# Performance work log

Hardware: AMD Instinct MI355X
Metric: run time of the kernel (lower is better)

Reference implementation:

```python
import jax, jax.numpy as jnp
import numpy as np

GROUPS = 8
MAX_DISP = 24
EPS = 1e-5


def group_norm(x, gamma, beta, groups):
    B, C = x.shape[0], x.shape[1]
    spatial = x.shape[2:]
    xg = x.reshape(B, groups, C // groups, -1)
    mean = xg.mean(axis=(2, 3), keepdims=True)
    var = xg.var(axis=(2, 3), keepdims=True)
    xn = ((xg - mean) * jax.lax.rsqrt(var + EPS)).reshape(B, C, *spatial)
    shp = (1, C) + (1,) * len(spatial)
    return xn * gamma.reshape(shp) + beta.reshape(shp)


def conv3d(x, w):
    return jax.lax.conv_general_dilated(x, w, (1, 1, 1), [(1, 1)] * 3,
                                        dimension_numbers=("NCDHW", "OIDHW", "NCDHW"))


def conv2d(x, w):
    return jax.lax.conv_general_dilated(x, w, (1, 1), [(1, 1)] * 2,
                                        dimension_numbers=("NCHW", "OIHW", "NCHW"))


def conv1d(x, w):
    return jax.lax.conv_general_dilated(x, w, (1,), [(1, 1)],
                                        dimension_numbers=("NCW", "OIW", "NCW"))


def setup_inputs() -> dict:
    key = jax.random.key(0)
    ks = jax.random.split(key, 12)
    B, C, H, W = 2, 64, 160, 320
    feat_out = 16
    fL = jax.random.normal(ks[0], (B, C, H, W), dtype=jnp.float32)
    fR = jax.random.normal(ks[1], (B, C, H, W), dtype=jnp.float32)
    def w(k, shape):
        fan_in = int(np.prod(shape[1:]))
        return jax.random.normal(k, shape, dtype=jnp.float32) / np.sqrt(fan_in)
    return {
        "fL": fL, "fR": fR,
        # agg: Conv3d(groups->16) GN SiLU, Conv3d(16->16) GN SiLU, Conv3d(16->1)+bias
        "agg_w1": w(ks[2], (16, GROUPS, 3, 3, 3)),
        "agg_g1": jnp.ones((16,), jnp.float32), "agg_b1": jnp.zeros((16,), jnp.float32),
        "agg_w2": w(ks[3], (16, 16, 3, 3, 3)),
        "agg_g2": jnp.ones((16,), jnp.float32), "agg_b2": jnp.zeros((16,), jnp.float32),
        "agg_w3": w(ks[4], (1, 16, 3, 3, 3)), "agg_bias3": jnp.zeros((1,), jnp.float32),
        # feat_head: Conv2d(C->feat_out) GN SiLU
        "feat_w": w(ks[5], (feat_out, C, 3, 3)),
        "feat_g": jnp.ones((feat_out,), jnp.float32), "feat_b": jnp.zeros((feat_out,), jnp.float32),
        # apc_d: Conv1d(max_disp->max_disp, k=3, no bias)
        "apc_w": w(ks[6], (MAX_DISP, MAX_DISP, 3)),
        "reg_w1": w(ks[7], (32, MAX_DISP + feat_out, 3, 3)),
        "reg_g1": jnp.ones((32,), jnp.float32), "reg_b1": jnp.zeros((32,), jnp.float32),
        "reg_w2": w(ks[8], (1, 32, 3, 3)), "reg_bias2": jnp.zeros((1,), jnp.float32),
    }


def reference(fL, fR, agg_w1, agg_g1, agg_b1, agg_w2, agg_g2, agg_b2,
              agg_w3, agg_bias3, feat_w, feat_g, feat_b, apc_w,
              reg_w1, reg_g1, reg_b1, reg_w2, reg_bias2):
    B, C, H, W = fL.shape
    G, D = GROUPS, MAX_DISP
    cg = C // G
    fL_g = fL.reshape(B, G, cg, H, W)

    # Cost volume: group-wise correlation with right feature shifted by d (zeros on left)
    def corr(d):
        fR_s = fR if d == 0 else jnp.pad(fR, ((0, 0), (0, 0), (0, 0), (d, 0)))[..., :W]
        return (fL_g * fR_s.reshape(B, G, cg, H, W)).mean(axis=2)  # [B,G,H,W]
    cv = jnp.stack([corr(d) for d in range(D)], axis=2)  # [B,G,D,H,W]

    # 3D aggregation
    h = jax.nn.silu(group_norm(conv3d(cv, agg_w1), agg_g1, agg_b1, 8))
    h = jax.nn.silu(group_norm(conv3d(h, agg_w2), agg_g2, agg_b2, 8))
    logits = (conv3d(h, agg_w3) + agg_bias3.reshape(1, 1, 1, 1, 1)).squeeze(1)  # [B,D,H,W]

    # Soft-argmin
    prob = jax.nn.softmax(logits, axis=1)
    disp_idx = jnp.arange(D, dtype=logits.dtype).reshape(1, D, 1, 1)
    d_sa = (prob * disp_idx).sum(axis=1, keepdims=True)  # [B,1,H,W]
    conf = prob.max(axis=1, keepdims=True)

    feat = jax.nn.silu(group_norm(conv2d(fL, feat_w), feat_g, feat_b, 8))  # [B,16,H,W]

    apc_out = conv1d(logits.reshape(B, D, H * W), apc_w).reshape(B, D, H, W)
    head_in = jnp.concatenate([apc_out, feat], axis=1)
    h2 = jax.nn.silu(group_norm(conv2d(head_in, reg_w1), reg_g1, reg_b1, 8))
    delta = conv2d(h2, reg_w2) + reg_bias2.reshape(1, 1, 1, 1)
    d_init = d_sa + delta

    sx = jnp.zeros_like(d_init)
    sy = jnp.zeros_like(d_init)
    return (d_init, sx, sy, feat, conf)
```

## Files before the change

kernel.cpp:

```cpp
#include <hip/hip_runtime.h>
#include <hip/hip_bf16.h>
#include <math.h>

constexpr int B_ = 2;
constexpr int C_ = 64;
constexpr int H_ = 160;
constexpr int W_ = 320;
constexpr int G_ = 8;
constexpr int D_ = 24;
constexpr int HW_ = H_ * W_;
constexpr int DHW_ = D_ * HW_;
constexpr float EPS_ = 1e-5f;

typedef __bf16 b8 __attribute__((ext_vector_type(8)));
typedef float  f4 __attribute__((ext_vector_type(4)));

__device__ inline float bf_lo(unsigned u) { return __builtin_bit_cast(float, u << 16); }
__device__ inline float bf_hi(unsigned u) { return __builtin_bit_cast(float, u & 0xffff0000u); }
__device__ inline unsigned pack2(float a, float b) {
  unsigned lo = __builtin_bit_cast(unsigned short, (__bf16)a);
  unsigned hi = __builtin_bit_cast(unsigned short, (__bf16)b);
  return (hi << 16) | lo;
}
__device__ inline float silu(float v) { return v / (1.f + __expf(-v)); }

__global__ __launch_bounds__(320)
void cv_cl_kernel(const float* __restrict__ fL, const float* __restrict__ fR,
                  __bf16* __restrict__ cv) {
  int w = threadIdx.x;
  int h = blockIdx.x % H_;
  int b = blockIdx.x / H_;
  int d0 = blockIdx.y * 6;
  const size_t rowbase = ((size_t)(b * C_) * H_ + h) * W_;
  float l[C_];
#pragma unroll
  for (int c = 0; c < C_; c++) l[c] = fL[rowbase + (size_t)c * HW_ + w];
  for (int dd = 0; dd < 6; dd++) {
    int d = d0 + dd;
    float s[8] = {0.f,0.f,0.f,0.f,0.f,0.f,0.f,0.f};
    if (w >= d) {
      const float* pr = fR + rowbase + (w - d);
#pragma unroll
      for (int c = 0; c < C_; c++) s[c >> 3] += l[c] * pr[(size_t)c * HW_];
    }
    b8 r;
#pragma unroll
    for (int g = 0; g < 8; g++) r[g] = (__bf16)(s[g] * 0.125f);
    *(b8*)(cv + ((size_t)((b * D_ + d) * H_ + h) * W_ + w) * 8) = r;
  }
}

__global__ void wprep_kernel(const float* __restrict__ w1, const float* __restrict__ w2,
                             __bf16* __restrict__ wf1, __bf16* __restrict__ wf2) {
  int lane = threadIdx.x;
  int co = lane & 15, kb = lane >> 4;
#pragma unroll
  for (int p = 0; p < 7; p++)
#pragma unroll
    for (int j = 0; j < 8; j++) {
      int kl = kb * 8 + j;
      int tap = p * 4 + (kl >> 3);
      int ci = kl & 7;
      float v = (tap <= 26) ? w1[(co * 8 + ci) * 27 + tap] : 0.f;
      wf1[(p * 64 + lane) * 8 + j] = (__bf16)v;
    }
#pragma unroll
  for (int p = 0; p < 14; p++)
#pragma unroll
    for (int j = 0; j < 8; j++) {
      int kl = kb * 8 + j;
      int tap = p * 2 + (kl >> 4);
      int ci = kl & 15;
      float v = (tap <= 26) ? w2[(co * 16 + ci) * 27 + tap] : 0.f;
      wf2[(p * 64 + lane) * 8 + j] = (__bf16)v;
    }
}

template <int CIN, int PAIRS>
__global__ __launch_bounds__(256)
void conv3d_mfma_kernel(const __bf16* __restrict__ in, const __bf16* __restrict__ wf,
                        __bf16* __restrict__ out) {
  const int lane = threadIdx.x & 63;
  const int wid = threadIdx.x >> 6;
  const int bid = blockIdx.x;
  const int h = bid % H_;
  const int d = (bid / H_) % D_;
  const int m = lane & 15;
  const int tpp = 32 / CIN;
  const int tapsel = (CIN == 16) ? (lane >> 5) : (lane >> 4);
  const int ci0 = (CIN == 16) ? ((lane >> 1) & 8) : 0;
  b8 wfr[PAIRS];
#pragma unroll
  for (int p = 0; p < PAIRS; p++) wfr[p] = *(const b8*)(wf + (p * 64 + lane) * 8);
  int poff[PAIRS], dwv[PAIRS];
  bool vdh[PAIRS];
#pragma unroll
  for (int p = 0; p < PAIRS; p++) {
    int tap = p * tpp + tapsel;
    if (tap > 26) tap = 26;
    int kd = tap / 9, kh = (tap / 3) % 3, kw = tap % 3;
    poff[p] = (kd - 1) * HW_ + (kh - 1) * W_ + (kw - 1);
    dwv[p] = kw - 1;
    vdh[p] = ((unsigned)(d + kd - 1) < (unsigned)D_) &&
             ((unsigned)(h + kh - 1) < (unsigned)H_);
  }
  const int pos0row = bid * W_;
  for (int t = 0; t < 5; t++) {
    const int w0 = (wid * 5 + t) * 16;
    const int pos0 = pos0row + w0;
    f4 acc = {0.f, 0.f, 0.f, 0.f};
#pragma unroll
    for (int p = 0; p < PAIRS; p++) {
      b8 a = {};
      if (vdh[p] && ((unsigned)(w0 + m + dwv[p]) < (unsigned)W_))
        a = *(const b8*)(in + (long)(pos0 + m + poff[p]) * CIN + ci0);
      acc = __builtin_amdgcn_mfma_f32_16x16x32_bf16(a, wfr[p], acc, 0, 0, 0);
    }
    const int co = lane & 15;
    const int r0 = (lane >> 4) * 4;
#pragma unroll
    for (int r = 0; r < 4; r++)
      out[(size_t)(pos0 + r0 + r) * 16 + co] = (__bf16)acc[r];
  }
}

__global__ __launch_bounds__(256)
void stats_cl_kernel(const __bf16* __restrict__ x, double* __restrict__ st) {
  int b = blockIdx.y;
  float sg[8] = {0,0,0,0,0,0,0,0}, sq[8] = {0,0,0,0,0,0,0,0};
  for (int i = blockIdx.x * 256 + threadIdx.x; i < DHW_; i += gridDim.x * 256) {
    const uint4* p = (const uint4*)(x + ((size_t)b * DHW_ + i) * 16);
    uint4 q0 = p[0], q1 = p[1];
    unsigned us[8] = {q0.x, q0.y, q0.z, q0.w, q1.x, q1.y, q1.z, q1.w};
#pragma unroll
    for (int k = 0; k < 8; k++) {
      float v0 = bf_lo(us[k]), v1 = bf_hi(us[k]);
      sg[k] += v0 + v1;
      sq[k] += v0 * v0 + v1 * v1;
    }
  }
#pragma unroll
  for (int k = 0; k < 8; k++)
    for (int off = 32; off; off >>= 1) {
      sg[k] += __shfl_xor(sg[k], off, 64);
      sq[k] += __shfl_xor(sq[k], off, 64);
    }
  __shared__ float ls[4][16];
  int wid = threadIdx.x >> 6, lane = threadIdx.x & 63;
  if (lane == 0) {
#pragma unroll
    for (int k = 0; k < 8; k++) { ls[wid][k] = sg[k]; ls[wid][8 + k] = sq[k]; }
  }
  __syncthreads();
  if (threadIdx.x < 16) {
    float t = ls[0][threadIdx.x] + ls[1][threadIdx.x] + ls[2][threadIdx.x] + ls[3][threadIdx.x];
    int g = threadIdx.x & 7, which = threadIdx.x >> 3;
    atomicAdd(&st[(size_t)(b * 8 + g) * 2 + which], (double)t);
  }
}

__global__ __launch_bounds__(256)
void norm_cl_kernel(__bf16* __restrict__ x, const double* __restrict__ st,
                    const float* __restrict__ gamma, const float* __restrict__ beta,
                    double invN) {
  int b = blockIdx.y;
  __shared__ float scs[16], shs[16];
  if (threadIdx.x < 16) {
    int c = threadIdx.x, grp = c >> 1;
    double mean = st[(size_t)(b * 8 + grp) * 2] * invN;
    double var = st[(size_t)(b * 8 + grp) * 2 + 1] * invN - mean * mean;
    float sc = gamma[c] * rsqrtf((float)var + EPS_);
    scs[c] = sc;
    shs[c] = beta[c] - (float)mean * sc;
  }
  __syncthreads();
  float sc[16], sh[16];
#pragma unroll
  for (int c = 0; c < 16; c++) { sc[c] = scs[c]; sh[c] = shs[c]; }
  for (int i = blockIdx.x * 256 + threadIdx.x; i < DHW_; i += gridDim.x * 256) {
    uint4* p = (uint4*)(x + ((size_t)b * DHW_ + i) * 16);
    uint4 q0 = p[0], q1 = p[1];
    unsigned us[8] = {q0.x, q0.y, q0.z, q0.w, q1.x, q1.y, q1.z, q1.w};
    unsigned ro[8];
#pragma unroll
    for (int k = 0; k < 8; k++) {
      int c0 = 2 * k;
      float v0 = silu(bf_lo(us[k]) * sc[c0] + sh[c0]);
      float v1 = silu(bf_hi(us[k]) * sc[c0 + 1] + sh[c0 + 1]);
      ro[k] = pack2(v0, v1);
    }
    p[0] = make_uint4(ro[0], ro[1], ro[2], ro[3]);
    p[1] = make_uint4(ro[4], ro[5], ro[6], ro[7]);
  }
}

__global__ __launch_bounds__(256)
void conv3_tile_kernel(const __bf16* __restrict__ a2, const float* __restrict__ wt,
                       const float* __restrict__ bias, float* __restrict__ logits) {
  __shared__ __align__(16) __bf16 li[5 * 6 * 2 * 66 * 8];
  __shared__ float lw[432];
  int bid = blockIdx.x;
  int wtile = bid % 5; bid /= 5;
  int ht = bid % 40; bid /= 40;
  int dt = bid % 8; bid /= 8;
  int b = bid;
  const int d0 = dt * 3, h0 = ht * 4, w0 = wtile * 64;
  for (int i = threadIdx.x; i < 432; i += 256) {
    int tap = i >> 4, ci = i & 15;
    lw[i] = wt[ci * 27 + tap];
  }
  for (int idx = threadIdx.x; idx < 5 * 6 * 66; idx += 256) {
    int pos = idx % 66;
    int r = idx / 66;
    int hh = r % 6, dd = r / 6;
    int d = d0 + dd - 1, h = h0 + hh - 1, w = w0 + pos - 1;
    uint4 v0 = make_uint4(0, 0, 0, 0), v1 = v0;
    if ((unsigned)d < (unsigned)D_ && (unsigned)h < (unsigned)H_ && (unsigned)w < (unsigned)W_) {
      const uint4* p = (const uint4*)(a2 + ((size_t)(((b * D_ + d) * H_ + h) * W_ + w)) * 16);
      v0 = p[0];
      v1 = p[1];
    }
    int vb = ((dd * 6 + hh) * 2) * 66 + pos;
    *(uint4*)(li + (size_t)vb * 8) = v0;
    *(uint4*)(li + (size_t)(vb + 66) * 8) = v1;
  }
  __syncthreads();
  const int ow = threadIdx.x & 63;
  const int oh = threadIdx.x >> 6;
  float acc[3] = {0.f, 0.f, 0.f};
  for (int kd = 0; kd < 3; kd++)
    for (int kh = 0; kh < 3; kh++)
      for (int kw = 0; kw < 3; kw++) {
        const int tap = kd * 9 + kh * 3 + kw;
        const float* wp = lw + tap * 16;
        float wv[16];
#pragma unroll
        for (int c = 0; c < 16; c++) wv[c] = wp[c];
        const int hh = oh + kh;
        const int pos = ow + kw;
#pragma unroll
        for (int od = 0; od < 3; od++) {
          const int dd = od + kd;
          const int vb = ((dd * 6 + hh) * 2) * 66 + pos;
          uint4 q0 = *(const uint4*)(li + (size_t)vb * 8);
          uint4 q1 = *(const uint4*)(li + (size_t)(vb + 66) * 8);
          acc[od] +=
            bf_lo(q0.x) * wv[0]  + bf_hi(q0.x) * wv[1]  + bf_lo(q0.y) * wv[2]  + bf_hi(q0.y) * wv[3] +
            bf_lo(q0.z) * wv[4]  + bf_hi(q0.z) * wv[5]  + bf_lo(q0.w) * wv[6]  + bf_hi(q0.w) * wv[7] +
            bf_lo(q1.x) * wv[8]  + bf_hi(q1.x) * wv[9]  + bf_lo(q1.y) * wv[10] + bf_hi(q1.y) * wv[11] +
            bf_lo(q1.z) * wv[12] + bf_hi(q1.z) * wv[13] + bf_lo(q1.w) * wv[14] + bf_hi(q1.w) * wv[15];
        }
      }
  const float bv = bias[0];
#pragma unroll
  for (int od = 0; od < 3; od++)
    logits[((size_t)(b * D_ + d0 + od) * H_ + (h0 + oh)) * W_ + w0 + ow] = acc[od] + bv;
}

template <int C0, int C1, int COUT, int COT, bool HASBIAS, bool ADD_DSA>
__global__ __launch_bounds__(320)
void conv2d_kernel(const float* __restrict__ in0, const float* __restrict__ in1,
                   const float* __restrict__ wt, const float* __restrict__ bias,
                   const float* __restrict__ dsa, float* __restrict__ out) {
  constexpr int CINT = C0 + C1;
  constexpr int CL = COUT / COT;
  __shared__ float lw[CL * CINT * 9];
  const int co0 = blockIdx.y * CL;
  for (int i = threadIdx.x; i < CL * CINT * 9; i += 320) lw[i] = wt[co0 * CINT * 9 + i];
  __syncthreads();
  int w = threadIdx.x;
  int h = blockIdx.x % H_;
  int b = blockIdx.x / H_;
  float acc[CL];
#pragma unroll
  for (int co = 0; co < CL; co++) acc[co] = 0.f;
  for (int kh = 0; kh < 3; kh++) {
    int hh = h + kh - 1;
    if (hh < 0 || hh >= H_) continue;
    for (int kw = 0; kw < 3; kw++) {
      int ww = w + kw - 1;
      if (ww < 0 || ww >= W_) continue;
#pragma unroll
      for (int ci = 0; ci < C0; ci++) {
        float v = in0[((size_t)(b * C0 + ci)) * HW_ + hh * W_ + ww];
        const float* lwp = lw + (ci * 3 + kh) * 3 + kw;
#pragma unroll
        for (int co = 0; co < CL; co++) acc[co] += v * lwp[co * CINT * 9];
      }
      if (C1 > 0) {
#pragma unroll
        for (int ci = 0; ci < (C1 > 0 ? C1 : 1); ci++) {
          float v = in1[((size_t)(b * C1 + ci)) * HW_ + hh * W_ + ww];
          const float* lwp = lw + ((C0 + ci) * 3 + kh) * 3 + kw;
#pragma unroll
          for (int co = 0; co < CL; co++) acc[co] += v * lwp[co * CINT * 9];
        }
      }
    }
  }
#pragma unroll
  for (int co = 0; co < CL; co++) {
    float r = acc[co];
    if (HASBIAS) r += bias[co0 + co];
    if (ADD_DSA) r += dsa[(size_t)b * HW_ + h * W_ + w];
    out[((size_t)(b * COUT + co0 + co)) * HW_ + h * W_ + w] = r;
  }
}

__global__ __launch_bounds__(256)
void conv1d_kernel(const float* __restrict__ logits, const float* __restrict__ wt,
                   float* __restrict__ out) {
  __shared__ float lw[D_ * D_ * 3];
  for (int i = threadIdx.x; i < D_ * D_ * 3; i += 256) lw[i] = wt[i];
  __syncthreads();
  int idx = blockIdx.x * 256 + threadIdx.x;
  int b = idx / HW_;
  int i = idx % HW_;
  float acc[D_];
#pragma unroll
  for (int o = 0; o < D_; o++) acc[o] = 0.f;
  for (int k = 0; k < 3; k++) {
    int pos = i + k - 1;
    if (pos < 0 || pos >= HW_) continue;
#pragma unroll
    for (int din = 0; din < D_; din++) {
      float v = logits[((size_t)b * D_ + din) * HW_ + pos];
      const float* lwp = lw + din * 3 + k;
#pragma unroll
      for (int o = 0; o < D_; o++) acc[o] += v * lwp[o * D_ * 3];
    }
  }
#pragma unroll
  for (int o = 0; o < D_; o++) out[((size_t)b * D_ + o) * HW_ + i] = acc[o];
}

__global__ __launch_bounds__(256)
void stats_kernel(const float* __restrict__ x, double* __restrict__ stats,
                  int Cc, int chg, size_t per_ch, int nchunk) {
  int tmp = blockIdx.x;
  int chunk = tmp % nchunk; tmp /= nchunk;
  int cig = tmp % chg; tmp /= chg;
  int grp = tmp % 8;
  int b = tmp / 8;
  int c = grp * chg + cig;
  size_t len = per_ch / nchunk;
  const float* p = x + ((size_t)b * Cc + c) * per_ch + (size_t)chunk * len;
  float s = 0.f, s2 = 0.f;
  for (size_t i = threadIdx.x; i < len; i += 256) {
    float v = p[i];
    s += v;
    s2 += v * v;
  }
  __shared__ double ls[256], ls2[256];
  ls[threadIdx.x] = (double)s;
  ls2[threadIdx.x] = (double)s2;
  __syncthreads();
  for (int off = 128; off > 0; off >>= 1) {
    if (threadIdx.x < off) {
      ls[threadIdx.x] += ls[threadIdx.x + off];
      ls2[threadIdx.x] += ls2[threadIdx.x + off];
    }
    __syncthreads();
  }
  if (threadIdx.x == 0) {
    atomicAdd(&stats[(size_t)(b * 8 + grp) * 2], ls[0]);
    atomicAdd(&stats[(size_t)(b * 8 + grp) * 2 + 1], ls2[0]);
  }
}

__global__ __launch_bounds__(256)
void norm_silu_f32o_kernel(const float* __restrict__ x, float* __restrict__ y,
                           const double* __restrict__ stats,
                           const float* __restrict__ gamma, const float* __restrict__ beta,
                           int chg, size_t per_ch, double invN) {
  int c = blockIdx.y;
  int b = blockIdx.z;
  int grp = c / chg;
  double s = stats[(size_t)(b * 8 + grp) * 2];
  double s2 = stats[(size_t)(b * 8 + grp) * 2 + 1];
  double mean_d = s * invN;
  double var_d = s2 * invN - mean_d * mean_d;
  float sc = gamma[c] / sqrtf((float)var_d + EPS_);
  float sh = beta[c] - (float)mean_d * sc;
  size_t base = ((size_t)b * gridDim.y + c) * per_ch;
  size_t chunk = (per_ch + gridDim.x - 1) / gridDim.x;
  size_t start = (size_t)blockIdx.x * chunk;
  size_t end = start + chunk;
  if (end > per_ch) end = per_ch;
  for (size_t i = start + threadIdx.x; i < end; i += 256) {
    float v = x[base + i] * sc + sh;
    y[base + i] = v / (1.f + __expf(-v));
  }
}

__global__ __launch_bounds__(320)
void softmax_kernel(const float* __restrict__ logits, float* __restrict__ dsa,
                    float* __restrict__ conf) {
  int w = threadIdx.x;
  int h = blockIdx.x % H_;
  int b = blockIdx.x / H_;
  size_t base = ((size_t)b * D_) * HW_ + h * W_ + w;
  float v[D_];
  float m = -1e30f;
#pragma unroll
  for (int d = 0; d < D_; d++) {
    v[d] = logits[base + (size_t)d * HW_];
    m = fmaxf(m, v[d]);
  }
  float s = 0.f, wd = 0.f;
#pragma unroll
  for (int d = 0; d < D_; d++) {
    float e = __expf(v[d] - m);
    s += e;
    wd += (float)d * e;
  }
  float inv = 1.f / s;
  dsa[(size_t)b * HW_ + h * W_ + w] = wd * inv;
  conf[(size_t)b * HW_ + h * W_ + w] = inv;
}


extern "C" void kernel_launch(void* const* d_in, const int* in_sizes, int n_in,
                              void* d_out, int out_size, void* d_ws, size_t ws_size,
                              hipStream_t stream) {
  const float* fL = (const float*)d_in[0];
  const float* fR = (const float*)d_in[1];
  const float* agg_w1 = (const float*)d_in[2];
  const float* agg_g1 = (const float*)d_in[3];
  const float* agg_b1 = (const float*)d_in[4];
  const float* agg_w2 = (const float*)d_in[5];
  const float* agg_g2 = (const float*)d_in[6];
  const float* agg_b2 = (const float*)d_in[7];
  const float* agg_w3 = (const float*)d_in[8];
  const float* agg_bias3 = (const float*)d_in[9];
  const float* feat_w = (const float*)d_in[10];
  const float* feat_g = (const float*)d_in[11];
  const float* feat_b = (const float*)d_in[12];
  const float* apc_w = (const float*)d_in[13];
  const float* reg_w1 = (const float*)d_in[14];
  const float* reg_g1 = (const float*)d_in[15];
  const float* reg_b1 = (const float*)d_in[16];
  const float* reg_w2 = (const float*)d_in[17];
  const float* reg_bias2 = (const float*)d_in[18];

  char* wsb = (char*)d_ws;
  constexpr size_t REG = 78643200ull;
  __bf16* a1 = (__bf16*)wsb;
  __bf16* cvb = (__bf16*)(wsb + REG);
  __bf16* a2 = (__bf16*)(wsb + REG);
  float* logits = (float*)wsb;
  float* apc = logits + 2457600;
  float* h2 = apc + 2457600;
  float* dsa = h2 + 3276800;
  float* featraw = dsa + 102400;
  __bf16* wf1 = (__bf16*)(wsb + 2 * REG);
  __bf16* wf2 = wf1 + 3584;
  double* stats = (double*)(wsb + 2 * REG + 21504);

  float* out = (float*)d_out;
  float* out_dinit = out;
  float* out_sx = out + 102400;
  float* out_feat = out + 307200;
  float* out_conf = out + 1945600;

  hipMemsetAsync(stats, 0, 128 * sizeof(double), stream);
  hipMemsetAsync(out_sx, 0, 2 * 102400 * sizeof(float), stream);

  wprep_kernel<<<1, 64, 0, stream>>>(agg_w1, agg_w2, wf1, wf2);

  cv_cl_kernel<<<dim3(B_ * H_, 4), 320, 0, stream>>>(fL, fR, cvb);

  conv3d_mfma_kernel<8, 7><<<B_ * D_ * H_, 256, 0, stream>>>(cvb, wf1, a1);
  stats_cl_kernel<<<dim3(256, B_), 256, 0, stream>>>(a1, stats + 0);
  norm_cl_kernel<<<dim3(512, B_), 256, 0, stream>>>(a1, stats + 0, agg_g1, agg_b1,
                                                    1.0 / (2.0 * DHW_));

  conv3d_mfma_kernel<16, 14><<<B_ * D_ * H_, 256, 0, stream>>>(a1, wf2, a2);
  stats_cl_kernel<<<dim3(256, B_), 256, 0, stream>>>(a2, stats + 32);
  norm_cl_kernel<<<dim3(512, B_), 256, 0, stream>>>(a2, stats + 32, agg_g2, agg_b2,
                                                    1.0 / (2.0 * DHW_));

  conv3_tile_kernel<<<3200, 256, 0, stream>>>(a2, agg_w3, agg_bias3, logits);

  softmax_kernel<<<B_ * H_, 320, 0, stream>>>(logits, dsa, out_conf);

  conv2d_kernel<C_, 0, 16, 2, false, false><<<dim3(B_ * H_, 2), 320, 0, stream>>>(
      fL, nullptr, feat_w, nullptr, nullptr, featraw);
  stats_kernel<<<B_ * 8 * 2 * 8, 256, 0, stream>>>(featraw, stats + 64, 16, 2, (size_t)HW_, 8);
  norm_silu_f32o_kernel<<<dim3(50, 16, B_), 256, 0, stream>>>(featraw, out_feat, stats + 64,
                                                              feat_g, feat_b, 2, (size_t)HW_,
                                                              1.0 / (2.0 * HW_));

  conv1d_kernel<<<(B_ * HW_) / 256, 256, 0, stream>>>(logits, apc_w, apc);

  conv2d_kernel<D_, 16, 32, 4, false, false><<<dim3(B_ * H_, 4), 320, 0, stream>>>(
      apc, out_feat, reg_w1, nullptr, nullptr, h2);
  stats_kernel<<<B_ * 8 * 4 * 8, 256, 0, stream>>>(h2, stats + 96, 32, 4, (size_t)HW_, 8);
  norm_silu_f32o_kernel<<<dim3(50, 32, B_), 256, 0, stream>>>(h2, h2, stats + 96, reg_g1, reg_b1,
                                                              4, (size_t)HW_, 1.0 / (4.0 * HW_));

  conv2d_kernel<32, 0, 1, 1, true, true><<<dim3(B_ * H_, 1), 320, 0, stream>>>(
      h2, nullptr, reg_w2, reg_bias2, dsa, out_dinit);
}
```

Before: 858.5 us.

## Stage conv3d input halo tile in LDS and split rows across blocks

The conv3d MFMA kernel now loads a 3x3x162 halo tile of the input into shared memory once per block, with zero padding, and reads all tap operands from LDS. Before, each of the 27 taps issued its own global gather with bounds checks. Each block now covers half a row (160 outputs) with 5 waves instead of a full row with 4 waves, and the grid doubles. This cuts redundant global loads and branch work, at the cost of a sync, LDS capacity pressure (up to about 47KB for CIN=16), and possible LDS bank conflicts.

```diff
diff --git a/kernel.cpp b/kernel.cpp
--- a/kernel.cpp
+++ b/kernel.cpp
@@ -77,14 +77,32 @@
 }
 
 template <int CIN, int PAIRS>
-__global__ __launch_bounds__(256)
+__global__ __launch_bounds__(320)
 void conv3d_mfma_kernel(const __bf16* __restrict__ in, const __bf16* __restrict__ wf,
                         __bf16* __restrict__ out) {
-  const int lane = threadIdx.x & 63;
-  const int wid = threadIdx.x >> 6;
-  const int bid = blockIdx.x;
+  __shared__ __align__(16) __bf16 li[9 * 162 * CIN];
+  const int tid = threadIdx.x;
+  int bid = blockIdx.x;
+  const int wt = bid & 1; bid >>= 1;
   const int h = bid % H_;
   const int d = (bid / H_) % D_;
+  const int b = bid / (H_ * D_);
+  const int w0 = wt * 160;
+  constexpr int VPE = CIN / 8;
+  for (int idx = tid; idx < 1458 * VPE; idx += 320) {
+    int entry = idx / VPE, half = idx % VPE;
+    int pos = entry % 162;
+    int r = entry / 162;
+    int hh = r % 3, dd = r / 3;
+    int dg = d + dd - 1, hg = h + hh - 1, wg = w0 + pos - 1;
+    uint4 v = make_uint4(0, 0, 0, 0);
+    if ((unsigned)dg < (unsigned)D_ && (unsigned)hg < (unsigned)H_ && (unsigned)wg < (unsigned)W_)
+      v = *(const uint4*)(in + ((size_t)((b * D_ + dg) * H_ + hg) * W_ + wg) * CIN + half * 8);
+    *(uint4*)(li + (size_t)entry * CIN + half * 8) = v;
+  }
+  __syncthreads();
+  const int lane = tid & 63;
+  const int wid = tid >> 6;
   const int m = lane & 15;
   const int tpp = 32 / CIN;
   const int tapsel = (CIN == 16) ? (lane >> 5) : (lane >> 4);
@@ -92,32 +110,27 @@
   b8 wfr[PAIRS];
 #pragma unroll
   for (int p = 0; p < PAIRS; p++) wfr[p] = *(const b8*)(wf + (p * 64 + lane) * 8);
-  int poff[PAIRS], dwv[PAIRS];
-  bool vdh[PAIRS];
+  int loff[PAIRS];
 #pragma unroll
   for (int p = 0; p < PAIRS; p++) {
     int tap = p * tpp + tapsel;
     if (tap > 26) tap = 26;
     int kd = tap / 9, kh = (tap / 3) % 3, kw = tap % 3;
-    poff[p] = (kd - 1) * HW_ + (kh - 1) * W_ + (kw - 1);
-    dwv[p] = kw - 1;
-    vdh[p] = ((unsigned)(d + kd - 1) < (unsigned)D_) &&
-             ((unsigned)(h + kh - 1) < (unsigned)H_);
-  }
-  const int pos0row = bid * W_;
-  for (int t = 0; t < 5; t++) {
-    const int w0 = (wid * 5 + t) * 16;
-    const int pos0 = pos0row + w0;
+    loff[p] = ((kd * 3 + kh) * 162 + kw) * CIN + ci0;
+  }
+  const int rowbase = ((b * D_ + d) * H_ + h) * W_ + w0;
+  for (int t = 0; t < 2; t++) {
+    const int m0 = (wid * 2 + t) * 16;
+    const int lbase = (m0 + m) * CIN;
     f4 acc = {0.f, 0.f, 0.f, 0.f};
 #pragma unroll
     for (int p = 0; p < PAIRS; p++) {
-      b8 a = {};
-      if (vdh[p] && ((unsigned)(w0 + m + dwv[p]) < (unsigned)W_))
-        a = *(const b8*)(in + (long)(pos0 + m + poff[p]) * CIN + ci0);
+      b8 a = *(const b8*)(li + lbase + loff[p]);
       acc = __builtin_amdgcn_mfma_f32_16x16x32_bf16(a, wfr[p], acc, 0, 0, 0);
     }
     const int co = lane & 15;
     const int r0 = (lane >> 4) * 4;
+    const int pos0 = rowbase + m0;
 #pragma unroll
     for (int r = 0; r < 4; r++)
       out[(size_t)(pos0 + r0 + r) * 16 + co] = (__bf16)acc[r];
@@ -470,12 +483,12 @@
 
   cv_cl_kernel<<<dim3(B_ * H_, 4), 320, 0, stream>>>(fL, fR, cvb);
 
-  conv3d_mfma_kernel<8, 7><<<B_ * D_ * H_, 256, 0, stream>>>(cvb, wf1, a1);
+  conv3d_mfma_kernel<8, 7><<<B_ * D_ * H_ * 2, 320, 0, stream>>>(cvb, wf1, a1);
   stats_cl_kernel<<<dim3(256, B_), 256, 0, stream>>>(a1, stats + 0);
   norm_cl_kernel<<<dim3(512, B_), 256, 0, stream>>>(a1, stats + 0, agg_g1, agg_b1,
                                                     1.0 / (2.0 * DHW_));
 
-  conv3d_mfma_kernel<16, 14><<<B_ * D_ * H_, 256, 0, stream>>>(a1, wf2, a2);
+  conv3d_mfma_kernel<16, 14><<<B_ * D_ * H_ * 2, 320, 0, stream>>>(a1, wf2, a2);
   stats_cl_kernel<<<dim3(256, B_), 256, 0, stream>>>(a2, stats + 32);
   norm_cl_kernel<<<dim3(512, B_), 256, 0, stream>>>(a2, stats + 32, agg_g2, agg_b2,
                                                     1.0 / (2.0 * DHW_));
```

Result: faster. 840.5 us (-2.1%).
